# Performance work log

Hardware: AMD Instinct MI355X
Metric: run time of the kernel (lower is better)

## Reference

```python
import jax, jax.numpy as jnp
import numpy as np

D = 1536          # model dim
N = 12            # num heads
HD = D // N       # head dim = 128
C = HD // 2       # rope complex channels = 64
F, H, W = 4, 32, 32
L = F * H * W     # 4096 tokens
B = 1
S1 = C - 2 * (C // 3)   # 22 channels for the frame axis
S2 = C // 3             # 21 channels each for h and w axes
EPS = 1e-6


def setup_inputs() -> dict:
    key = jax.random.key(0)
    ks = jax.random.split(key, 9)
    sc = 1.0 / np.sqrt(D)
    inp = {"x": jax.random.normal(ks[0], (B, L, D), jnp.float32)}
    for i, name in enumerate(["wq", "wk", "wv", "wo"]):
        inp[name] = jax.random.normal(ks[1 + i], (D, D), jnp.float32) * sc
    for i, name in enumerate(["bq", "bk", "bv", "bo"]):
        inp[name] = jax.random.normal(ks[5 + i], (D,), jnp.float32) * 0.01
    inp["gq"] = jnp.ones((D,), jnp.float32)
    inp["gk"] = jnp.ones((D,), jnp.float32)
    # precomputed rotary tables: angle[pos, j] = pos * theta_j (complex freqs = cos + i sin)
    pos = jnp.arange(1024, dtype=jnp.float32)
    inv = 10000.0 ** (-jnp.arange(C, dtype=jnp.float32) / C)
    ang = pos[:, None] * inv[None, :]
    inp["freqs_cos"] = jnp.cos(ang)
    inp["freqs_sin"] = jnp.sin(ang)
    inp["seq_lens"] = jnp.full((B,), L, dtype=jnp.int32)
    inp["f_size"] = F
    inp["h_size"] = H
    inp["w_size"] = W
    return inp


def _rms(y, g):
    return y * jax.lax.rsqrt(jnp.mean(y * y, axis=-1, keepdims=True) + EPS) * g


def _grid(tab, f, h, w):
    # concat per-axis frequency bands: [f,h,w, S1 | S2 | rest] -> [L, 1, C]
    a = jnp.broadcast_to(tab[:f, None, None, :S1], (f, h, w, S1))
    b = jnp.broadcast_to(tab[None, :h, None, S1:S1 + S2], (f, h, w, S2))
    c = jnp.broadcast_to(tab[None, None, :w, S1 + S2:], (f, h, w, C - S1 - S2))
    return jnp.concatenate([a, b, c], axis=-1).reshape(f * h * w, 1, C)


def reference(x, wq, bq, wk, bk, wv, bv, wo, bo, gq, gk,
              freqs_cos, freqs_sin, seq_lens, f_size, h_size, w_size):
    b, l, dim = x.shape
    n = N
    d = dim // n
    c = d // 2
    # QKV projections with QK RMSNorm (norm over full model dim, as in the module)
    q = _rms(x @ wq.T + bq, gq).reshape(b, l, n, d)
    k = _rms(x @ wk.T + bk, gk).reshape(b, l, n, d)
    v = (x @ wv.T + bv).reshape(b, l, n, d)
    # 3D rotary: complex multiply by per-position grid frequencies
    cosg = _grid(freqs_cos, f_size, h_size, w_size)  # [L,1,C]
    sing = _grid(freqs_sin, f_size, h_size, w_size)

    def rope(t):
        tr = t.reshape(b, l, n, c, 2)
        xr, xi = tr[..., 0], tr[..., 1]
        return jnp.stack([xr * cosg - xi * sing, xr * sing + xi * cosg], axis=-1).reshape(b, l, n, d)

    q = rope(q)
    k = rope(k)
    # full (non-windowed) scaled dot-product attention, all k_lens == L
    scores = jnp.einsum('blnd,bmnd->bnlm', q, k) / jnp.sqrt(jnp.float32(d))
    attn = jax.nn.softmax(scores, axis=-1)
    out = jnp.einsum('bnlm,bmnd->blnd', attn, v).reshape(b, l, dim)
    return out @ wo.T + bo
```

## Files before the change

kernel.cpp:

```cpp
#include <hip/hip_runtime.h>
#include <math.h>

#define Dm   1536
#define NHd  12
#define HDm  128
#define Ltok 4096
#define S1c  22
#define S2c  21
#define MFIX 5.0f

typedef __attribute__((ext_vector_type(8))) _Float16 f16x8;
typedef __attribute__((ext_vector_type(4))) float f32x4;

static __device__ __forceinline__ f32x4 MFMA16(f16x8 a, f16x8 b, f32x4 c) {
  return __builtin_amdgcn_mfma_f32_16x16x32_f16(a, b, c, 0, 0, 0);
}

static __device__ __forceinline__ unsigned int pack_f16(float a, float b) {
  union { _Float16 h[2]; unsigned int u; } x;
  x.h[0] = (_Float16)a; x.h[1] = (_Float16)b;
  return x.u;
}

static __device__ __forceinline__ void gload_lds16(const void* g, void* l) {
  __builtin_amdgcn_global_load_lds(
      (const __attribute__((address_space(1))) unsigned int*)g,
      (__attribute__((address_space(3))) unsigned int*)l, 16, 0, 0);
}

__global__ __launch_bounds__(256) void cvt_f16(
    const float* __restrict__ src, unsigned short* __restrict__ dst, int nslots)
{
  int i = blockIdx.x * 256 + threadIdx.x;
  if (i >= nslots) return;
  float4 v = *(const float4*)&src[(size_t)i * 4];
  uint2 p;
  p.x = pack_f16(v.x, v.y);
  p.y = pack_f16(v.z, v.w);
  *(uint2*)&dst[(size_t)i * 4] = p;
}

__global__ __launch_bounds__(256) void cvt_w4_f16(
    const float* __restrict__ w0, const float* __restrict__ w1,
    const float* __restrict__ w2, const float* __restrict__ w3,
    unsigned short* __restrict__ dst)
{
  const int which = blockIdx.y;
  const float* src = (which == 0) ? w0 : (which == 1) ? w1 : (which == 2) ? w2 : w3;
  unsigned short* d = dst + (size_t)which * Dm * Dm;
  int i = blockIdx.x * 256 + threadIdx.x;
  float4 v = *(const float4*)&src[(size_t)i * 4];
  uint2 p;
  p.x = pack_f16(v.x, v.y);
  p.y = pack_f16(v.z, v.w);
  *(uint2*)&d[(size_t)i * 4] = p;
}

__global__ __launch_bounds__(256) void gemm_qkv_f16(
    const unsigned short* __restrict__ Ag, const unsigned short* __restrict__ Wg,
    const float* __restrict__ bq, const float* __restrict__ bk,
    const float* __restrict__ bv,
    float* __restrict__ qb, float* __restrict__ kb,
    unsigned short* __restrict__ vT)
{
  __shared__ __align__(16) unsigned short As[128][32], Bs[128][32];
  const int tid = threadIdx.x;
  const int w = tid >> 6, lane = tid & 63;
  const int nx = lane & 15, g = lane >> 4;
  const int m0 = blockIdx.y * 128, n0 = blockIdx.x * 128;
  const int wr = w >> 1, wc = w & 1;
  const int which = (n0 >= 2 * Dm) ? 2 : ((n0 >= Dm) ? 1 : 0);
  const int n0loc = n0 - which * Dm;

  const int srow = lane >> 2, scol = (lane & 3) * 8;
  const unsigned short* gp;
  char* lbase;
  if (w < 2) {
    gp = Ag + (size_t)(m0 + w * 64 + srow) * Dm + scol;
    lbase = (char*)&As[0][0] + w * 4096;
  } else {
    gp = Wg + (size_t)(n0 + (w - 2) * 64 + srow) * Dm + scol;
    lbase = (char*)&Bs[0][0] + (w - 2) * 4096;
  }

  f32x4 acc[4][4];
#pragma unroll
  for (int i = 0; i < 4; i++)
#pragma unroll
    for (int j = 0; j < 4; j++) acc[i][j] = (f32x4){0.f, 0.f, 0.f, 0.f};

  for (int it = 0; it < Dm / 32; ++it) {
    __syncthreads();
#pragma unroll
    for (int c = 0; c < 4; ++c)
      gload_lds16(gp + (size_t)c * 16 * Dm, lbase + c * 1024);
    gp += 32;
    __syncthreads();
    f16x8 ah[4], bh[4];
#pragma unroll
    for (int i = 0; i < 4; ++i) {
      ah[i] = *(const f16x8*)&As[wr * 64 + i * 16 + nx][g * 8];
      bh[i] = *(const f16x8*)&Bs[wc * 64 + i * 16 + nx][g * 8];
    }
#pragma unroll
    for (int i = 0; i < 4; ++i)
#pragma unroll
      for (int j = 0; j < 4; ++j)
        acc[i][j] = MFMA16(ah[i], bh[j], acc[i][j]);
  }

  if (which < 2) {
    float* Cout = which ? kb : qb;
    const float* bias = which ? bk : bq;
#pragma unroll
    for (int j = 0; j < 4; ++j) {
      const int col = n0loc + wc * 64 + j * 16 + nx;
      const float bz = bias[col];
#pragma unroll
      for (int i = 0; i < 4; ++i) {
        const int row0 = m0 + wr * 64 + i * 16 + g * 4;
#pragma unroll
        for (int r = 0; r < 4; ++r)
          Cout[(size_t)(row0 + r) * Dm + col] = acc[i][j][r] + bz;
      }
    }
  } else {
#pragma unroll
    for (int j = 0; j < 4; ++j) {
      const int col = n0loc + wc * 64 + j * 16 + nx;
      const float bz = bv[col];
#pragma unroll
      for (int i = 0; i < 4; ++i) {
        const int row0 = m0 + wr * 64 + i * 16 + g * 4;
        uint2 pk;
        pk.x = pack_f16(acc[i][j][0] + bz, acc[i][j][1] + bz);
        pk.y = pack_f16(acc[i][j][2] + bz, acc[i][j][3] + bz);
        *(uint2*)&vT[(size_t)col * Ltok + row0] = pk;
      }
    }
  }
}

__global__ __launch_bounds__(256) void gemm_nt_f16(
    const unsigned short* __restrict__ Ag, const unsigned short* __restrict__ Wg,
    const float* __restrict__ bias, float* __restrict__ Cout)
{
  __shared__ __align__(16) unsigned short As[128][32], Bs[128][32];
  const int tid = threadIdx.x;
  const int w = tid >> 6, lane = tid & 63;
  const int nx = lane & 15, g = lane >> 4;
  const int m0 = blockIdx.y * 128, n0 = blockIdx.x * 128;
  const int wr = w >> 1, wc = w & 1;

  const int srow = lane >> 2, scol = (lane & 3) * 8;
  const unsigned short* gp;
  char* lbase;
  if (w < 2) {
    gp = Ag + (size_t)(m0 + w * 64 + srow) * Dm + scol;
    lbase = (char*)&As[0][0] + w * 4096;
  } else {
    gp = Wg + (size_t)(n0 + (w - 2) * 64 + srow) * Dm + scol;
    lbase = (char*)&Bs[0][0] + (w - 2) * 4096;
  }

  f32x4 acc[4][4];
#pragma unroll
  for (int i = 0; i < 4; i++)
#pragma unroll
    for (int j = 0; j < 4; j++) acc[i][j] = (f32x4){0.f, 0.f, 0.f, 0.f};

  for (int it = 0; it < Dm / 32; ++it) {
    __syncthreads();
#pragma unroll
    for (int c = 0; c < 4; ++c)
      gload_lds16(gp + (size_t)c * 16 * Dm, lbase + c * 1024);
    gp += 32;
    __syncthreads();
    f16x8 ah[4], bh[4];
#pragma unroll
    for (int i = 0; i < 4; ++i) {
      ah[i] = *(const f16x8*)&As[wr * 64 + i * 16 + nx][g * 8];
      bh[i] = *(const f16x8*)&Bs[wc * 64 + i * 16 + nx][g * 8];
    }
#pragma unroll
    for (int i = 0; i < 4; ++i)
#pragma unroll
      for (int j = 0; j < 4; ++j)
        acc[i][j] = MFMA16(ah[i], bh[j], acc[i][j]);
  }
#pragma unroll
  for (int j = 0; j < 4; ++j) {
    const int col = n0 + wc * 64 + j * 16 + nx;
    const float bz = bias[col];
#pragma unroll
    for (int i = 0; i < 4; ++i) {
      const int row0 = m0 + wr * 64 + i * 16 + g * 4;
#pragma unroll
      for (int r = 0; r < 4; ++r)
        Cout[(size_t)(row0 + r) * Dm + col] = acc[i][j][r] + bz;
    }
  }
}

__global__ __launch_bounds__(256) void rmsnorm_rope_f16(
    float* __restrict__ q, float* __restrict__ k,
    const float* __restrict__ gq, const float* __restrict__ gk,
    const float* __restrict__ fcos, const float* __restrict__ fsin)
{
  const int l = blockIdx.x;
  const int tid = threadIdx.x;
  const int d0 = tid * 6;
  float qv[6], kv[6];
  float sq = 0.f, sk = 0.f;
  const float* qp = &q[(size_t)l * Dm + d0];
  const float* kp = &k[(size_t)l * Dm + d0];
#pragma unroll
  for (int i = 0; i < 6; i++) {
    qv[i] = qp[i]; sq += qv[i] * qv[i];
    kv[i] = kp[i]; sk += kv[i] * kv[i];
  }
#pragma unroll
  for (int s = 1; s < 64; s <<= 1) {
    sq += __shfl_xor(sq, s);
    sk += __shfl_xor(sk, s);
  }
  __shared__ float redq[4], redk[4];
  if ((tid & 63) == 0) { redq[tid >> 6] = sq; redk[tid >> 6] = sk; }
  __syncthreads();
  sq = redq[0] + redq[1] + redq[2] + redq[3];
  sk = redk[0] + redk[1] + redk[2] + redk[3];
  const float rq = rsqrtf(sq * (1.f / (float)Dm) + 1e-6f);
  const float rk = rsqrtf(sk * (1.f / (float)Dm) + 1e-6f);
  const float qscale = 0.08838834764831845f;
  const int f = l >> 10, h = (l >> 5) & 31, w = l & 31;
  unsigned short* qo = (unsigned short*)q + (size_t)l * Dm;
  unsigned short* ko = (unsigned short*)k + (size_t)l * Dm;
#pragma unroll
  for (int i = 0; i < 3; i++) {
    const int d = d0 + 2 * i;
    const int cc = (d & (HDm - 1)) >> 1;
    const int pos = (cc < S1c) ? f : ((cc < S1c + S2c) ? h : w);
    const float co = fcos[pos * 64 + cc];
    const float si = fsin[pos * 64 + cc];
    const float xr = qv[2 * i]     * rq * gq[d];
    const float xi = qv[2 * i + 1] * rq * gq[d + 1];
    *(unsigned int*)&qo[d] =
        pack_f16((xr * co - xi * si) * qscale, (xr * si + xi * co) * qscale);
    const float yr = kv[2 * i]     * rk * gk[d];
    const float yi = kv[2 * i + 1] * rk * gk[d + 1];
    *(unsigned int*)&ko[d] = pack_f16(yr * co - yi * si, yr * si + yi * co);
  }
}

__global__ __launch_bounds__(256, 3) void attn_f16(
    const unsigned short* __restrict__ qs, const unsigned short* __restrict__ ks,
    const unsigned short* __restrict__ vT,
    float* __restrict__ Op0, float* __restrict__ Op1,
    float* __restrict__ stats)
{
  __shared__ __align__(16) unsigned short Ks[2][32][136];
  __shared__ __align__(16) unsigned short Vs[2][128][40];
  __shared__ __align__(16) unsigned short Ps[4][32][40];

  const int tid = threadIdx.x;
  const int w = tid >> 6, lane = tid & 63;
  const int nx = lane & 15, g = lane >> 4;
  const int head = blockIdx.y;
  const int half = blockIdx.z;
  const int qbase = blockIdx.x * 128 + w * 32;
  const int kvbase = half * (Ltok / 2);
  float* __restrict__ Op = half ? Op1 : Op0;

  f16x8 qf[2][4];
#pragma unroll
  for (int s = 0; s < 2; s++) {
    const unsigned short* qp =
        &qs[(size_t)(qbase + s * 16 + nx) * Dm + head * HDm + g * 8];
#pragma unroll
    for (int c = 0; c < 4; c++) qf[s][c] = *(const f16x8*)(qp + c * 32);
  }

  f32x4 oacc[2][8];
#pragma unroll
  for (int s = 0; s < 2; s++)
#pragma unroll
    for (int nt = 0; nt < 8; nt++) oacc[s][nt] = (f32x4){0.f, 0.f, 0.f, 0.f};
  float lrow[2] = {0.f, 0.f};

  const int krow = tid >> 3, kchb = (tid & 7) << 4;
  const int vrow = tid >> 1, vseg = (tid & 1) << 4;

  const unsigned short* kg = &ks[(size_t)(kvbase + krow) * Dm + head * HDm + kchb];
  const unsigned short* vg = &vT[((size_t)head * HDm + vrow) * Ltok + kvbase + vseg];

  {
    uint4 ka = *(const uint4*)kg, kb4 = *(const uint4*)(kg + 8);
    uint4 va = *(const uint4*)vg, vb4 = *(const uint4*)(vg + 8);
    *(uint4*)&Ks[0][krow][kchb]     = ka;
    *(uint4*)&Ks[0][krow][kchb + 8] = kb4;
    *(uint4*)&Vs[0][vrow][vseg]     = va;
    *(uint4*)&Vs[0][vrow][vseg + 8] = vb4;
  }
  __syncthreads();

  const int NIT = Ltok / 2 / 32;
  for (int t = 0; t < NIT; t++) {
    const int cur = t & 1, nxt = cur ^ 1;
    const bool pref = (t + 1 < NIT);
    uint4 ka, kb4, va, vb4;
    if (pref) {
      kg += 32 * Dm;
      vg += 32;
      ka  = *(const uint4*)kg;  kb4 = *(const uint4*)(kg + 8);
      va  = *(const uint4*)vg;  vb4 = *(const uint4*)(vg + 8);
    }

    f32x4 sa[2][2];
#pragma unroll
    for (int s = 0; s < 2; s++)
#pragma unroll
      for (int mt = 0; mt < 2; mt++) sa[s][mt] = (f32x4){0.f, 0.f, 0.f, 0.f};
#pragma unroll
    for (int c = 0; c < 4; c++) {
      f16x8 k0f = *(const f16x8*)&Ks[cur][nx][c * 32 + g * 8];
      f16x8 k1f = *(const f16x8*)&Ks[cur][16 + nx][c * 32 + g * 8];
#pragma unroll
      for (int s = 0; s < 2; s++) {
        sa[s][0] = MFMA16(k0f, qf[s][c], sa[s][0]);
        sa[s][1] = MFMA16(k1f, qf[s][c], sa[s][1]);
      }
    }

#pragma unroll
    for (int s = 0; s < 2; s++) {
      float p[8], ps = 0.f;
#pragma unroll
      for (int r = 0; r < 4; r++) {
        p[r]     = __expf(sa[s][0][r] - MFIX);
        p[4 + r] = __expf(sa[s][1][r] - MFIX);
      }
#pragma unroll
      for (int j = 0; j < 8; j++) ps += p[j];
      ps += __shfl_xor(ps, 16);
      ps += __shfl_xor(ps, 32);
      lrow[s] += ps;
#pragma unroll
      for (int mt = 0; mt < 2; mt++) {
        unsigned int u0 = pack_f16(p[4 * mt + 0], p[4 * mt + 1]);
        unsigned int u1 = pack_f16(p[4 * mt + 2], p[4 * mt + 3]);
        *(uint2*)&Ps[w][s * 16 + nx][mt * 16 + g * 4] = make_uint2(u0, u1);
      }
    }
    __builtin_amdgcn_sched_barrier(0);

    f16x8 ph[2];
#pragma unroll
    for (int s = 0; s < 2; s++)
      ph[s] = *(const f16x8*)&Ps[w][s * 16 + nx][g * 8];
#pragma unroll
    for (int nt = 0; nt < 8; nt++) {
      f16x8 vh = *(const f16x8*)&Vs[cur][nt * 16 + nx][g * 8];
#pragma unroll
      for (int s = 0; s < 2; s++)
        oacc[s][nt] = MFMA16(ph[s], vh, oacc[s][nt]);
    }

    if (pref) {
      *(uint4*)&Ks[nxt][krow][kchb]     = ka;
      *(uint4*)&Ks[nxt][krow][kchb + 8] = kb4;
      *(uint4*)&Vs[nxt][vrow][vseg]     = va;
      *(uint4*)&Vs[nxt][vrow][vseg + 8] = vb4;
    }
    __syncthreads();
  }

#pragma unroll
  for (int s = 0; s < 2; s++) {
#pragma unroll
    for (int nt = 0; nt < 8; nt++)
#pragma unroll
      for (int r = 0; r < 4; r++)
        Op[(size_t)(qbase + s * 16 + g * 4 + r) * Dm + head * HDm + nt * 16 + nx] =
            oacc[s][nt][r];
    if (g == 0)
      stats[((size_t)half * Ltok + qbase + s * 16 + nx) * NHd + head] = lrow[s];
  }
}

__global__ __launch_bounds__(384) void combine_f16(
    const float* __restrict__ Op0, const float* __restrict__ Op1,
    const float* __restrict__ stats, unsigned short* __restrict__ oh)
{
  const int row = blockIdx.x;
  const int c4 = threadIdx.x * 4;
  const int head = c4 >> 7;
  const float l0 = stats[(size_t)row * NHd + head];
  const float l1 = stats[((size_t)Ltok + row) * NHd + head];
  const float rl = 1.f / (l0 + l1);
  float4 o0 = *(const float4*)&Op0[(size_t)row * Dm + c4];
  float4 o1 = *(const float4*)&Op1[(size_t)row * Dm + c4];
  uint2 p;
  p.x = pack_f16((o0.x + o1.x) * rl, (o0.y + o1.y) * rl);
  p.y = pack_f16((o0.z + o1.z) * rl, (o0.w + o1.w) * rl);
  *(uint2*)&oh[(size_t)row * Dm + c4] = p;
}

extern "C" void kernel_launch(void* const* d_in, const int* in_sizes, int n_in,
                              void* d_out, int out_size, void* d_ws, size_t ws_size,
                              hipStream_t stream)
{
  const float* x    = (const float*)d_in[0];
  const float* wq   = (const float*)d_in[1];
  const float* wk   = (const float*)d_in[2];
  const float* wv   = (const float*)d_in[3];
  const float* wo   = (const float*)d_in[4];
  const float* bq   = (const float*)d_in[5];
  const float* bk   = (const float*)d_in[6];
  const float* bv   = (const float*)d_in[7];
  const float* bo   = (const float*)d_in[8];
  const float* gq   = (const float*)d_in[9];
  const float* gk   = (const float*)d_in[10];
  const float* fcos = (const float*)d_in[11];
  const float* fsin = (const float*)d_in[12];
  float* out = (float*)d_out;

  const size_t LD = (size_t)Ltok * Dm;
  const size_t WH = (size_t)Dm * Dm;
  float* base = (float*)d_ws;
  float* qb = base;
  float* kb = base + LD;
  unsigned short* vT  = (unsigned short*)(base + 2 * LD);
  unsigned short* xh  = (unsigned short*)(base + 2 * LD + LD / 2);
  float* Op0 = base + 2 * LD + LD / 2;
  float* Op1 = Op0 + LD;
  unsigned short* wqh = (unsigned short*)(Op1 + LD);
  unsigned short* woh = wqh + 3 * WH;
  unsigned short* oh  = (unsigned short*)base;
  float* stats = (float*)(wqh + 4 * WH);

  const int xslots = (int)(LD / 4);
  const int w4     = (int)(WH / 4);
  dim3 gqkv(3 * Dm / 128, Ltok / 128);
  dim3 gout(Dm / 128, Ltok / 128);

  cvt_f16<<<(xslots + 255) / 256, 256, 0, stream>>>(x, xh, xslots);
  cvt_w4_f16<<<dim3(w4 / 256, 4), 256, 0, stream>>>(wq, wk, wv, wo, wqh);

  gemm_qkv_f16<<<gqkv, 256, 0, stream>>>(xh, wqh, bq, bk, bv, qb, kb, vT);
  rmsnorm_rope_f16<<<Ltok, 256, 0, stream>>>(qb, kb, gq, gk, fcos, fsin);
  attn_f16<<<dim3(Ltok / 128, NHd, 2), 256, 0, stream>>>(
      (const unsigned short*)qb, (const unsigned short*)kb, vT, Op0, Op1, stats);
  combine_f16<<<Ltok, 384, 0, stream>>>(Op0, Op1, stats, oh);
  gemm_nt_f16<<<gout, 256, 0, stream>>>(oh, woh, bo, out);
}
```

Before: 417.5 us.

## Fold softmax row-sum into MFMA via ones row; use exp2 with prescaled Q

Pre-multiplies the Q scale by log2(e) and seeds the score accumulators with the fixed shift, so the softmax exponent becomes a bare exp2. The per-row probability sum is no longer done with adds and cross-lane shuffles; instead a ones row is appended to the V tile in shared memory, and an extra MFMA output tile accumulates the row sums. This removes VALU and shuffle work per iteration, at the cost of one extra MFMA pair per step, more shared memory and more accumulator registers, which could affect occupancy. The row sums are accumulated from the f16-rounded probabilities, which changes the rounding slightly.

```diff
diff --git a/kernel.cpp b/kernel.cpp
--- a/kernel.cpp
+++ b/kernel.cpp
@@ -8,6 +8,7 @@
 #define S1c  22
 #define S2c  21
 #define MFIX 5.0f
+#define LOG2E 1.4426950408889634f
 
 typedef __attribute__((ext_vector_type(8))) _Float16 f16x8;
 typedef __attribute__((ext_vector_type(4))) float f32x4;
@@ -231,7 +232,7 @@
   sk = redk[0] + redk[1] + redk[2] + redk[3];
   const float rq = rsqrtf(sq * (1.f / (float)Dm) + 1e-6f);
   const float rk = rsqrtf(sk * (1.f / (float)Dm) + 1e-6f);
-  const float qscale = 0.08838834764831845f;
+  const float qscale = 0.08838834764831845f * LOG2E;
   const int f = l >> 10, h = (l >> 5) & 31, w = l & 31;
   unsigned short* qo = (unsigned short*)q + (size_t)l * Dm;
   unsigned short* ko = (unsigned short*)k + (size_t)l * Dm;
@@ -259,7 +260,7 @@
     float* __restrict__ stats)
 {
   __shared__ __align__(16) unsigned short Ks[2][32][136];
-  __shared__ __align__(16) unsigned short Vs[2][128][40];
+  __shared__ __align__(16) unsigned short Vs[2][144][40];
   __shared__ __align__(16) unsigned short Ps[4][32][40];
 
   const int tid = threadIdx.x;
@@ -271,6 +272,15 @@
   const int kvbase = half * (Ltok / 2);
   float* __restrict__ Op = half ? Op1 : Op0;
 
+  const float NEGMFIX2 = -MFIX * LOG2E;
+
+  for (int i = tid; i < 2 * 16 * 40; i += 256) {
+    const int b = i / 640, rem = i - b * 640;
+    const int r = rem / 40, cc = rem - r * 40;
+    Vs[b][128 + r][cc] =
+        (r == 0 && cc < 32) ? (unsigned short)0x3C00 : (unsigned short)0;
+  }
+
   f16x8 qf[2][4];
 #pragma unroll
   for (int s = 0; s < 2; s++) {
@@ -280,12 +290,11 @@
     for (int c = 0; c < 4; c++) qf[s][c] = *(const f16x8*)(qp + c * 32);
   }
 
-  f32x4 oacc[2][8];
+  f32x4 oacc[2][9];
 #pragma unroll
   for (int s = 0; s < 2; s++)
 #pragma unroll
-    for (int nt = 0; nt < 8; nt++) oacc[s][nt] = (f32x4){0.f, 0.f, 0.f, 0.f};
-  float lrow[2] = {0.f, 0.f};
+    for (int nt = 0; nt < 9; nt++) oacc[s][nt] = (f32x4){0.f, 0.f, 0.f, 0.f};
 
   const int krow = tid >> 3, kchb = (tid & 7) << 4;
   const int vrow = tid >> 1, vseg = (tid & 1) << 4;
@@ -319,7 +328,8 @@
 #pragma unroll
     for (int s = 0; s < 2; s++)
 #pragma unroll
-      for (int mt = 0; mt < 2; mt++) sa[s][mt] = (f32x4){0.f, 0.f, 0.f, 0.f};
+      for (int mt = 0; mt < 2; mt++)
+        sa[s][mt] = (f32x4){NEGMFIX2, NEGMFIX2, NEGMFIX2, NEGMFIX2};
 #pragma unroll
     for (int c = 0; c < 4; c++) {
       f16x8 k0f = *(const f16x8*)&Ks[cur][nx][c * 32 + g * 8];
@@ -333,17 +343,12 @@
 
 #pragma unroll
     for (int s = 0; s < 2; s++) {
-      float p[8], ps = 0.f;
+      float p[8];
 #pragma unroll
       for (int r = 0; r < 4; r++) {
-        p[r]     = __expf(sa[s][0][r] - MFIX);
-        p[4 + r] = __expf(sa[s][1][r] - MFIX);
+        p[r]     = exp2f(sa[s][0][r]);
+        p[4 + r] = exp2f(sa[s][1][r]);
       }
-#pragma unroll
-      for (int j = 0; j < 8; j++) ps += p[j];
-      ps += __shfl_xor(ps, 16);
-      ps += __shfl_xor(ps, 32);
-      lrow[s] += ps;
 #pragma unroll
       for (int mt = 0; mt < 2; mt++) {
         unsigned int u0 = pack_f16(p[4 * mt + 0], p[4 * mt + 1]);
@@ -358,7 +363,7 @@
     for (int s = 0; s < 2; s++)
       ph[s] = *(const f16x8*)&Ps[w][s * 16 + nx][g * 8];
 #pragma unroll
-    for (int nt = 0; nt < 8; nt++) {
+    for (int nt = 0; nt < 9; nt++) {
       f16x8 vh = *(const f16x8*)&Vs[cur][nt * 16 + nx][g * 8];
 #pragma unroll
       for (int s = 0; s < 2; s++)
@@ -382,8 +387,12 @@
       for (int r = 0; r < 4; r++)
         Op[(size_t)(qbase + s * 16 + g * 4 + r) * Dm + head * HDm + nt * 16 + nx] =
             oacc[s][nt][r];
-    if (g == 0)
-      stats[((size_t)half * Ltok + qbase + s * 16 + nx) * NHd + head] = lrow[s];
+    if (nx == 0) {
+#pragma unroll
+      for (int r = 0; r < 4; r++)
+        stats[((size_t)half * Ltok + qbase + s * 16 + g * 4 + r) * NHd + head] =
+            oacc[s][8][r];
+    }
   }
 }
 
```

Result: no change. 416.1 us (-0.3%).
